# Kernel optimization log

Measured on AMD Instinct MI355X. Metric: run time of the kernel, lower is better.

Reference implementation:

```python
import jax, jax.numpy as jnp
import numpy as np

B, N, H, D = 16, 128, 32, 5            # graphs, entities, heads, multi_hop_max_dist
NUM_EDGES, NUM_SPATIAL, NUM_EDGE_DIS = 1536, 512, 128
HID, NEF = 768, 3                       # hidden dim (unused in math), edge feats


def setup_inputs() -> dict:
    key = jax.random.key(0)
    ks = jax.random.split(key, 8)
    x = jax.random.normal(ks[0], (B, N, HID), jnp.float32)
    attn_bias = jax.random.normal(ks[1], (B, N + 1, N + 1), jnp.float32)
    spatial_pos = jax.random.randint(ks[2], (B, N, N), 0, NUM_SPATIAL)
    edge_input = jax.random.randint(ks[3], (B, N, N, D, NEF), 0, NUM_EDGES + 1)
    # embedding tables (std=0.02 init; padding_idx=0 rows zeroed)
    edge_encoder_w = (0.02 * jax.random.normal(ks[4], (NUM_EDGES + 1, H), jnp.float32)).at[0].set(0.0)
    structural_w = (0.02 * jax.random.normal(ks[5], (NUM_SPATIAL, H), jnp.float32)).at[0].set(0.0)
    edge_dis_w = 0.02 * jax.random.normal(ks[6], (NUM_EDGE_DIS * H * H, 1), jnp.float32)
    virt_w = 0.02 * jax.random.normal(ks[7], (1, H), jnp.float32)
    return {"x": x, "attn_bias": attn_bias, "spatial_pos": spatial_pos,
            "edge_input": edge_input, "edge_encoder_w": edge_encoder_w,
            "structural_w": structural_w, "edge_dis_w": edge_dis_w, "virt_w": virt_w}


def reference(x, attn_bias, spatial_pos, edge_input, edge_encoder_w, structural_w, edge_dis_w, virt_w):
    n_graph, n_entity = x.shape[:2]
    # [B, H, N+1, N+1]
    bias = jnp.broadcast_to(attn_bias[:, None], (n_graph, H, n_entity + 1, n_entity + 1))
    # structural (spatial) encoding on the NxN sub-block
    sp_bias = structural_w[spatial_pos].transpose(0, 3, 1, 2)          # [B,H,N,N]
    bias = bias.at[:, :, 1:, 1:].add(sp_bias)
    # graph-token virtual distance
    t = virt_w.reshape(1, H, 1)
    bias = bias.at[:, :, 1:, 0].add(t)
    bias = bias.at[:, :, 0, :].add(t)
    # ---- multi_hop relational encoding ----
    sp = jnp.where(spatial_pos == 0, 1, spatial_pos)
    sp = jnp.where(sp > 1, sp - 1, sp)
    sp = jnp.clip(sp, 0, D)                                            # [B,N,N]
    ei = edge_input[:, :, :, :D, :]                                    # [B,N,N,D,F]
    ei = edge_encoder_w[ei].mean(-2)                                   # [B,N,N,D,H]
    # per-hop head-mixing: bmm over hop dim
    Wdis = edge_dis_w.reshape(-1, H, H)[:D]                            # [D,H,H]
    ei = jnp.einsum('bijdh,dhk->bijdk', ei, Wdis)                      # [B,N,N,D,H]
    ei = ei.sum(-2) / sp[..., None].astype(ei.dtype)                   # [B,N,N,H]
    ei = ei.transpose(0, 3, 1, 2)                                      # [B,H,N,N]
    bias = bias.at[:, :, 1:, 1:].add(ei)
    # final residual add of raw attn_bias
    bias = bias + attn_bias[:, None]
    return bias
```

## Files before the change

kernel.cpp:

```cpp
#include <hip/hip_runtime.h>

#define B_   16
#define N_   128
#define H_   32
#define D_   5
#define NEF_ 3
#define NE1  1537
#define NP1  129

__global__ __launch_bounds__(256) void fused_tab_kernel(
    const float* __restrict__ edge_encoder_w,
    const float* __restrict__ edge_dis_w,
    float* __restrict__ fused)
{
    __shared__ float wd[32 * 32];
    const int tid = threadIdx.x;
    const int bx  = blockIdx.x;
    const int d     = bx / 193;
    const int chunk = bx % 193;

    const float* wsrc = edge_dis_w + d * 1024;
    for (int k = tid; k < 1024; k += 256) wd[k] = wsrc[k];
    __syncthreads();

    const int g    = tid >> 5;
    const int lane = tid & 31;
    const int idx  = chunk * 8 + g;
    if (idx >= NE1) return;

    float w = edge_encoder_w[idx * 32 + lane];
    float acc = 0.f;
    #pragma unroll
    for (int hh = 0; hh < 32; ++hh) {
        acc += __shfl(w, hh, 32) * wd[hh * 32 + lane];
    }
    fused[(d * NE1 + idx) * 32 + lane] = acc;
}

__global__ __launch_bounds__(256) void main_kernel(
    const float* __restrict__ attn_bias,
    const int*   __restrict__ spatial_pos,
    const int*   __restrict__ edge_input,
    const float* __restrict__ structural_w,
    const float* __restrict__ fused,
    float* __restrict__ out)
{
    __shared__ float tile[32][33];

    const int bx  = blockIdx.x;
    const int jt  = bx & 3;
    const int i   = (bx >> 2) & 127;
    const int b   = bx >> 9;
    const int tid  = threadIdx.x;
    const int g    = tid >> 5;
    const int lane = tid & 31;

    #pragma unroll
    for (int jj = 0; jj < 4; ++jj) {
        const int jl = g * 4 + jj;
        const int j  = jt * 32 + jl;
        const int cell = (b * N_ + i) * N_ + j;

        const int* eip = edge_input + cell * (D_ * NEF_);
        int my_idx = (lane < 15) ? eip[lane] : 0;
        const int sp0 = spatial_pos[cell];

        float acc = 0.f;
        #pragma unroll
        for (int t = 0; t < 15; ++t) {
            const int id = __shfl(my_idx, t, 32);
            const int d  = t / 3;
            acc += fused[(d * NE1 + id) * 32 + lane];
        }

        int s = sp0;
        if (s == 0) s = 1;
        if (s > 1)  s -= 1;
        if (s > D_) s = D_;

        float val = acc / (3.0f * (float)s) + structural_w[sp0 * 32 + lane];
        tile[lane][jl] = val;
    }
    __syncthreads();

    const int j = jt * 32 + lane + 1;
    const float ab2 = 2.0f * attn_bias[(b * NP1 + (i + 1)) * NP1 + j];
    #pragma unroll
    for (int rr = 0; rr < 4; ++rr) {
        const int h = g + rr * 8;
        out[((b * H_ + h) * NP1 + (i + 1)) * NP1 + j] = ab2 + tile[h][lane];
    }
}

__global__ __launch_bounds__(256) void border_kernel(
    const float* __restrict__ attn_bias,
    const float* __restrict__ virt_w,
    float* __restrict__ out)
{
    const int bh = blockIdx.x;
    const int b = bh >> 5;
    const int h = bh & 31;
    const float t = virt_w[h];

    float*       ob = out + (b * H_ + h) * NP1 * NP1;
    const float* ab = attn_bias + b * NP1 * NP1;

    for (int idx = threadIdx.x; idx < NP1 + N_; idx += 256) {
        if (idx < NP1) {
            ob[idx] = 2.0f * ab[idx] + t;
        } else {
            const int i = idx - 128;
            ob[i * NP1] = 2.0f * ab[i * NP1] + t;
        }
    }
}

extern "C" void kernel_launch(void* const* d_in, const int* in_sizes, int n_in,
                              void* d_out, int out_size, void* d_ws, size_t ws_size,
                              hipStream_t stream) {
    const float* attn_bias      = (const float*)d_in[1];
    const int*   spatial_pos    = (const int*)  d_in[2];
    const int*   edge_input     = (const int*)  d_in[3];
    const float* edge_encoder_w = (const float*)d_in[4];
    const float* structural_w   = (const float*)d_in[5];
    const float* edge_dis_w     = (const float*)d_in[6];
    const float* virt_w         = (const float*)d_in[7];
    float* out   = (float*)d_out;
    float* fused = (float*)d_ws;

    hipLaunchKernelGGL(fused_tab_kernel, dim3(5 * 193), dim3(256), 0, stream,
                       edge_encoder_w, edge_dis_w, fused);
    hipLaunchKernelGGL(main_kernel, dim3(B_ * N_ * 4), dim3(256), 0, stream,
                       attn_bias, spatial_pos, edge_input, structural_w, fused, out);
    hipLaunchKernelGGL(border_kernel, dim3(B_ * H_), dim3(256), 0, stream,
                       attn_bias, virt_w, out);
}
```

Measured before the change: 119.6 us.

## Store fused edge table in bf16 and remap main kernel to wave64 lanes

The precomputed fused edge-encoder/head-mixing table is now stored in bfloat16, halving its footprint and gather traffic in the main kernel. The main kernel is also remapped to 64-lane wavefronts, with 4 waves each handling 8 cells, and uses readfirstlane/readlane scalar broadcasts instead of shuffles. Only the low 32 lanes of each wave do the gather, so half the lanes sit idle during it. bf16 rounding adds numerical error to the bias output, which may matter against a tight tolerance.

Result: slower. 135.6 us (+13.4%).

```diff
diff --git a/kernel.cpp b/kernel.cpp
--- a/kernel.cpp
+++ b/kernel.cpp
@@ -1,4 +1,5 @@
 #include <hip/hip_runtime.h>
+#include <hip/hip_bf16.h>
 
 #define B_   16
 #define N_   128
@@ -11,7 +12,7 @@
 __global__ __launch_bounds__(256) void fused_tab_kernel(
     const float* __restrict__ edge_encoder_w,
     const float* __restrict__ edge_dis_w,
-    float* __restrict__ fused)
+    __hip_bfloat16* __restrict__ fused)
 {
     __shared__ float wd[32 * 32];
     const int tid = threadIdx.x;
@@ -34,7 +35,7 @@
     for (int hh = 0; hh < 32; ++hh) {
         acc += __shfl(w, hh, 32) * wd[hh * 32 + lane];
     }
-    fused[(d * NE1 + idx) * 32 + lane] = acc;
+    fused[(d * NE1 + idx) * 32 + lane] = __float2bfloat16(acc);
 }
 
 __global__ __launch_bounds__(256) void main_kernel(
@@ -42,53 +43,60 @@
     const int*   __restrict__ spatial_pos,
     const int*   __restrict__ edge_input,
     const float* __restrict__ structural_w,
-    const float* __restrict__ fused,
+    const __hip_bfloat16* __restrict__ fused,
     float* __restrict__ out)
 {
     __shared__ float tile[32][33];
 
-    const int bx  = blockIdx.x;
-    const int jt  = bx & 3;
-    const int i   = (bx >> 2) & 127;
-    const int b   = bx >> 9;
+    const int bx   = blockIdx.x;
+    const int jt   = bx & 3;
+    const int i    = (bx >> 2) & 127;
+    const int b    = bx >> 9;
     const int tid  = threadIdx.x;
-    const int g    = tid >> 5;
-    const int lane = tid & 31;
+    const int wave = tid >> 6;
+    const int lane = tid & 63;
+    const int h    = lane & 31;
 
     #pragma unroll
-    for (int jj = 0; jj < 4; ++jj) {
-        const int jl = g * 4 + jj;
+    for (int jj = 0; jj < 8; ++jj) {
+        const int jl = wave * 8 + jj;
         const int j  = jt * 32 + jl;
-        const int cell = (b * N_ + i) * N_ + j;
+        int cell = (b * N_ + i) * N_ + j;
+        cell = __builtin_amdgcn_readfirstlane(cell);
 
+        const int sp0 = spatial_pos[cell];
         const int* eip = edge_input + cell * (D_ * NEF_);
-        int my_idx = (lane < 15) ? eip[lane] : 0;
-        const int sp0 = spatial_pos[cell];
+        int idx_v = 0;
+        if (lane < 15) idx_v = eip[lane];
 
-        float acc = 0.f;
-        #pragma unroll
-        for (int t = 0; t < 15; ++t) {
-            const int id = __shfl(my_idx, t, 32);
-            const int d  = t / 3;
-            acc += fused[(d * NE1 + id) * 32 + lane];
+        if (lane < 32) {
+            float acc = 0.f;
+            #pragma unroll
+            for (int t = 0; t < 15; ++t) {
+                const int id = __builtin_amdgcn_readlane(idx_v, t);
+                const int d  = t / 3;
+                const __hip_bfloat16* row = fused + (d * NE1 + id) * 32;
+                acc += __bfloat162float(row[h]);
+            }
+            int s = sp0;
+            if (s == 0) s = 1;
+            if (s > 1)  s -= 1;
+            if (s > D_) s = D_;
+            const float val = acc / (3.0f * (float)s)
+                            + structural_w[sp0 * 32 + h];
+            tile[h][jl] = val;
         }
-
-        int s = sp0;
-        if (s == 0) s = 1;
-        if (s > 1)  s -= 1;
-        if (s > D_) s = D_;
-
-        float val = acc / (3.0f * (float)s) + structural_w[sp0 * 32 + lane];
-        tile[lane][jl] = val;
     }
     __syncthreads();
 
-    const int j = jt * 32 + lane + 1;
+    const int g2    = tid >> 5;
+    const int lane2 = tid & 31;
+    const int j = jt * 32 + lane2 + 1;
     const float ab2 = 2.0f * attn_bias[(b * NP1 + (i + 1)) * NP1 + j];
     #pragma unroll
     for (int rr = 0; rr < 4; ++rr) {
-        const int h = g + rr * 8;
-        out[((b * H_ + h) * NP1 + (i + 1)) * NP1 + j] = ab2 + tile[h][lane];
+        const int hh = g2 + rr * 8;
+        out[((b * H_ + hh) * NP1 + (i + 1)) * NP1 + j] = ab2 + tile[hh][lane2];
     }
 }
 
@@ -125,8 +133,8 @@
     const float* structural_w   = (const float*)d_in[5];
     const float* edge_dis_w     = (const float*)d_in[6];
     const float* virt_w         = (const float*)d_in[7];
-    float* out   = (float*)d_out;
-    float* fused = (float*)d_ws;
+    float* out = (float*)d_out;
+    __hip_bfloat16* fused = (__hip_bfloat16*)d_ws;
 
     hipLaunchKernelGGL(fused_tab_kernel, dim3(5 * 193), dim3(256), 0, stream,
                        edge_encoder_w, edge_dis_w, fused);
```
